# Kernel tuning notes

Measured on AMD Instinct MI355X. Metric: run time of the kernel, lower is better.

## Reference

```python
import math
import jax, jax.numpy as jnp
import numpy as np

B, T, N, F, H = 8, 16, 64, 64, 1024  # feature_dim must equal num_regions for the einsum to be valid


def _linear_init(key, out_dim, in_dim):
    kw, kb = jax.random.split(key)
    s = 1.0 / np.sqrt(in_dim)
    W = jax.random.uniform(kw, (out_dim, in_dim), jnp.float32, -s, s)
    b = jax.random.uniform(kb, (out_dim,), jnp.float32, -s, s)
    return W, b


def setup_inputs() -> dict:
    key = jax.random.key(0)
    k0, k1, k2, k3, k4 = jax.random.split(key, 5)
    M = jax.random.normal(k0, (B, T, N, N, F), jnp.float32)
    Wo, bo = _linear_init(k1, H, N * F)      # origin_proj
    Wso, bso = _linear_init(k2, N, H)        # origin_score
    Wd, bd = _linear_init(k3, H, N * F)      # dest_proj
    Wsd, bsd = _linear_init(k4, N, H)        # dest_score
    return {"M": M, "Wo": Wo, "bo": bo, "Wso": Wso, "bso": bso,
            "Wd": Wd, "bd": bd, "Wsd": Wsd, "bsd": bsd}


def _sparse_attention(scores, u):
    # scores: (BT, N, N)
    p = jax.nn.softmax(scores, axis=-1)
    entropy = -jnp.sum(p * jnp.log(p + 1e-9), axis=-1)          # (BT, N)
    _, top_idx = jax.lax.top_k(-entropy, u)                      # u smallest-entropy rows
    bt = entropy.shape[0]
    mask = jnp.zeros(entropy.shape, bool).at[jnp.arange(bt)[:, None], top_idx].set(True)
    return p * mask[..., None]                                   # zero all but u rows


def reference(M, Wo, bo, Wso, bso, Wd, bd, Wsd, bsd):
    Bb, Tt, Nn, _, Ff = M.shape
    BT = Bb * Tt
    X = M.reshape(BT, Nn, Nn * Ff)                               # origin view
    Y = jnp.transpose(M, (0, 1, 3, 2, 4)).reshape(BT, Nn, Nn * Ff)  # dest view
    omega_scores = (X @ Wo.T + bo) @ Wso.T + bso                 # (BT, N, N)
    delta_scores = (Y @ Wd.T + bd) @ Wsd.T + bsd                 # (BT, N, N)
    u = max(1, int(math.log(Nn)))
    omega = _sparse_attention(omega_scores, u)
    delta = _sparse_attention(delta_scores, u)
    M_flat = M.reshape(BT, Nn, Nn, Ff)
    out = jnp.einsum('bij,bjkl->bikl', omega, M_flat)            # (BT, N, N, F)
    out = jnp.einsum('bikl,bjl->bijk', out, delta)               # requires F == N
    return out.reshape(Bb, Tt, Nn, Nn, Ff)
```

## Files before the change

kernel.cpp:

```cpp
#include <hip/hip_runtime.h>
#include <math.h>

#define NB 8
#define NT 16
#define NN 64
#define NF 64
#define NH 1024
#define BT 128
#define NFK 4096

typedef float  f32x4 __attribute__((ext_vector_type(4)));
typedef short  s16x8 __attribute__((ext_vector_type(8)));

#define MFMA_B16(a, b, c) __builtin_amdgcn_mfma_f32_16x16x32_bf16(a, b, c, 0, 0, 0)

#define BEFF_FOFF   524288
#define PSEL_FOFF   524416
#define RTAB_FOFF   589952
#define RES_FOFF    606336
#define DYN_FOFF    737408

__device__ __forceinline__ void split_bf16(float v, unsigned short& hi, unsigned short& lo) {
    unsigned u = __float_as_uint(v);
    float r = v - __uint_as_float(u & 0xFFFF0000u);
    hi = (unsigned short)(u >> 16);
    lo = (unsigned short)(__float_as_uint(r) >> 16);
}

__device__ __forceinline__ void split8(const float4& a0, const float4& a1, s16x8& ah, s16x8& al) {
    float fa[8];
    *(float4*)&fa[0] = a0; *(float4*)&fa[4] = a1;
    #pragma unroll
    for (int j = 0; j < 8; ++j) {
        unsigned u = __float_as_uint(fa[j]);
        float r = fa[j] - __uint_as_float(u & 0xFFFF0000u);
        ah[j] = (short)(u >> 16);
        al[j] = (short)(__float_as_uint(r) >> 16);
    }
}

__global__ __launch_bounds__(256) void fold_part(
    const float* __restrict__ Wso, const float* __restrict__ Wo,
    const float* __restrict__ Wsd, const float* __restrict__ Wd,
    float* __restrict__ fpart, int hchunk)
{
    const int which = blockIdx.y, kc = blockIdx.z;
    const float* __restrict__ A  = which ? Wsd : Wso;
    const float* __restrict__ Bm = which ? Wd  : Wo;
    const int c0 = blockIdx.x * 32;

    __shared__ float As[64][68];
    __shared__ float Bs[32][68];

    const int t = threadIdx.x;
    const int tx = t & 7, ty = t >> 3;

    float acc[2][4] = {};

    const int h0beg = kc * hchunk, h0end = h0beg + hchunk;
    for (int h0 = h0beg; h0 < h0end; h0 += 64) {
        #pragma unroll
        for (int it = 0; it < 4; ++it) {
            int r = (t >> 4) + it * 16, c4 = (t & 15) * 4;
            *(float4*)&As[r][c4] = *(const float4*)&A[r * NH + h0 + c4];
        }
        #pragma unroll
        for (int it = 0; it < 2; ++it) {
            int h = (t >> 3) + it * 32, cq = t & 7;
            float4 v = *(const float4*)&Bm[(size_t)(h0 + h) * NFK + c0 + cq * 4];
            Bs[cq * 4 + 0][h] = v.x; Bs[cq * 4 + 1][h] = v.y;
            Bs[cq * 4 + 2][h] = v.z; Bs[cq * 4 + 3][h] = v.w;
        }
        __syncthreads();
        #pragma unroll 4
        for (int kk = 0; kk < 64; kk += 4) {
            float4 a4[2], b4[4];
            a4[0] = *(const float4*)&As[ty][kk];
            a4[1] = *(const float4*)&As[ty + 32][kk];
            #pragma unroll
            for (int n = 0; n < 4; ++n) b4[n] = *(const float4*)&Bs[tx + 8 * n][kk];
            #pragma unroll
            for (int m = 0; m < 2; ++m)
                #pragma unroll
                for (int n = 0; n < 4; ++n)
                    acc[m][n] += a4[m].x * b4[n].x + a4[m].y * b4[n].y
                               + a4[m].z * b4[n].z + a4[m].w * b4[n].w;
        }
        __syncthreads();
    }
    float* __restrict__ outp = fpart + ((size_t)(kc * 2 + which) * 64) * NFK;
    #pragma unroll
    for (int m = 0; m < 2; ++m)
        #pragma unroll
        for (int n = 0; n < 4; ++n)
            outp[(size_t)(ty + 32 * m) * NFK + c0 + tx + 8 * n] = acc[m][n];
}

__global__ __launch_bounds__(256) void fold_reduce(
    const float* __restrict__ fpart, unsigned short* __restrict__ wfrag, int fcc)
{
    const int which = blockIdx.y;
    const int c0 = blockIdx.x * 64;
    const int t = threadIdx.x;
    const int r = t >> 2, cb = (t & 3) * 16;

    float s[16] = {};
    for (int c = 0; c < fcc; ++c) {
        const float* __restrict__ p =
            fpart + ((size_t)(c * 2 + which) * 64 + r) * NFK + c0 + cb;
        #pragma unroll
        for (int qq = 0; qq < 4; ++qq) {
            float4 v = *(const float4*)(p + 4 * qq);
            s[4 * qq + 0] += v.x; s[4 * qq + 1] += v.y;
            s[4 * qq + 2] += v.z; s[4 * qq + 3] += v.w;
        }
    }
    #pragma unroll
    for (int jj = 0; jj < 16; ++jj) {
        int c = c0 + cb + jj;
        unsigned short hi, lo;
        split_bf16(s[jj], hi, lo);
        int ct = r >> 4, lane = (((c >> 3) & 3) << 4) | (r & 15);
        int ks = c >> 5, j = c & 7;
        size_t offh = ((((size_t)(which * 2 + 0) * 4 + ct) * 128 + ks) * 64 + lane) * 8 + j;
        size_t offl = ((((size_t)(which * 2 + 1) * 4 + ct) * 128 + ks) * 64 + lane) * 8 + j;
        wfrag[offh] = hi;
        wfrag[offl] = lo;
    }
}

__global__ __launch_bounds__(256) void bias_kernel(
    const float* __restrict__ Wso, const float* __restrict__ bo, const float* __restrict__ bso,
    const float* __restrict__ Wsd, const float* __restrict__ bd, const float* __restrict__ bsd,
    float* __restrict__ beff)
{
    const int which = blockIdx.x;
    const float* __restrict__ Ws = which ? Wsd : Wso;
    const float* __restrict__ bb = which ? bd  : bo;
    const float* __restrict__ bs = which ? bsd : bso;
    const int t = threadIdx.x;
    const int r = t >> 2, c = t & 3;
    const float* wp = Ws + r * NH + c * 256;
    const float* bp = bb + c * 256;
    float s = 0.f;
    #pragma unroll 4
    for (int i = 0; i < 64; ++i) {
        float4 wv = *(const float4*)(wp + 4 * i);
        float4 bv = *(const float4*)(bp + 4 * i);
        s += wv.x * bv.x + wv.y * bv.y + wv.z * bv.z + wv.w * bv.w;
    }
    __shared__ float part[64][4];
    part[r][c] = s;
    __syncthreads();
    if (t < 64)
        beff[which * 64 + t] = bs[t] + part[t][0] + part[t][1] + part[t][2] + part[t][3];
}

__global__ __launch_bounds__(256) void scores_part(
    const float* __restrict__ M, const unsigned short* __restrict__ wfrag,
    float* __restrict__ spart, int ksc)
{
    const int bt = blockIdx.x, which = blockIdx.y, kc = blockIdx.z;
    const float* __restrict__ Mbt = M + (size_t)bt * NN * NN * NF;
    const int t = threadIdx.x;
    const int w = t >> 6, l = t & 63, q = l >> 4, ln = l & 15;
    const int arow = 16 * w + ln;

    const unsigned short* __restrict__ wfl = wfrag + (size_t)which * 524288 + (size_t)l * 8;
#define BOFF(part, ct, ks) ((((part) * 4 + (ct)) * 128 + (ks)) * 512)
#define AADDR(ks) (Mbt + q * 8 + ((which == 0) \
        ? (arow * NFK + (ks) * 32) \
        : ((((ks) >> 1) * NFK) + arow * 64 + (((ks) & 1) * 32))))

    const int ks0 = kc * ksc, ksend = ks0 + ksc;
    const int g0 = ks0 >> 2, gend = ksend >> 2;

    f32x4 acc[4];
    #pragma unroll
    for (int ct = 0; ct < 4; ++ct) acc[ct] = (f32x4)0.f;

    float4 Ac[4][2], An[4][2];
    #pragma unroll
    for (int kk = 0; kk < 4; ++kk) {
        const float* ap = AADDR(ks0 + kk);
        Ac[kk][0] = *(const float4*)ap;
        Ac[kk][1] = *(const float4*)(ap + 4);
    }
    s16x8 bhc[4], blc[4];
    #pragma unroll
    for (int ct = 0; ct < 4; ++ct) {
        bhc[ct] = *(const s16x8*)(wfl + BOFF(0, ct, ks0));
        blc[ct] = *(const s16x8*)(wfl + BOFF(1, ct, ks0));
    }

    for (int g = g0; g < gend; ++g) {
        if (g + 1 < gend) {
            #pragma unroll
            for (int kk = 0; kk < 4; ++kk) {
                const float* ap = AADDR(4 * (g + 1) + kk);
                An[kk][0] = *(const float4*)ap;
                An[kk][1] = *(const float4*)(ap + 4);
            }
        }
        #pragma unroll
        for (int kk = 0; kk < 4; ++kk) {
            const int ks = 4 * g + kk;
            s16x8 bhn[4], bln[4];
            const bool pf = (ks + 1 < ksend);
            if (pf) {
                #pragma unroll
                for (int ct = 0; ct < 4; ++ct) {
                    bhn[ct] = *(const s16x8*)(wfl + BOFF(0, ct, ks + 1));
                    bln[ct] = *(const s16x8*)(wfl + BOFF(1, ct, ks + 1));
                }
            }
            s16x8 ah, al;
            split8(Ac[kk][0], Ac[kk][1], ah, al);
            #pragma unroll
            for (int ct = 0; ct < 4; ++ct) {
                acc[ct] = MFMA_B16(ah, bhc[ct], acc[ct]);
                acc[ct] = MFMA_B16(al, bhc[ct], acc[ct]);
                acc[ct] = MFMA_B16(ah, blc[ct], acc[ct]);
            }
            if (pf) {
                #pragma unroll
                for (int ct = 0; ct < 4; ++ct) { bhc[ct] = bhn[ct]; blc[ct] = bln[ct]; }
            }
        }
        #pragma unroll
        for (int kk = 0; kk < 4; ++kk) { Ac[kk][0] = An[kk][0]; Ac[kk][1] = An[kk][1]; }
    }
#undef AADDR
#undef BOFF

    float* __restrict__ pout = spart + ((size_t)(kc * 2 + which) * BT + bt) * 4096;
    #pragma unroll
    for (int ct = 0; ct < 4; ++ct)
        #pragma unroll
        for (int reg = 0; reg < 4; ++reg)
            pout[(16 * w + 4 * q + reg) * 64 + 16 * ct + ln] = acc[ct][reg];
}

__global__ __launch_bounds__(256) void finalize_kernel(
    const float* __restrict__ spart, const float* __restrict__ beff,
    float* __restrict__ psel, int* __restrict__ rtab, int scc)
{
    const int bt = blockIdx.x, which = blockIdx.y;
    const int t = threadIdx.x;
    const int row = t >> 2, cb = (t & 3) * 16;

    float s[16] = {};
    for (int c = 0; c < scc; ++c) {
        const float* __restrict__ p =
            spart + ((size_t)(c * 2 + which) * BT + bt) * 4096 + row * 64 + cb;
        #pragma unroll
        for (int qq = 0; qq < 4; ++qq) {
            float4 v = *(const float4*)(p + 4 * qq);
            s[4 * qq + 0] += v.x; s[4 * qq + 1] += v.y;
            s[4 * qq + 2] += v.z; s[4 * qq + 3] += v.w;
        }
    }
    #pragma unroll
    for (int jj = 0; jj < 16; ++jj) s[jj] += beff[which * 64 + cb + jj];

    float m = -INFINITY;
    #pragma unroll
    for (int jj = 0; jj < 16; ++jj) m = fmaxf(m, s[jj]);
    m = fmaxf(m, __shfl_xor(m, 1));
    m = fmaxf(m, __shfl_xor(m, 2));

    float e[16], sum = 0.f;
    #pragma unroll
    for (int jj = 0; jj < 16; ++jj) { e[jj] = expf(s[jj] - m); sum += e[jj]; }
    sum += __shfl_xor(sum, 1);
    sum += __shfl_xor(sum, 2);
    const float inv = 1.0f / sum;

    float pv[16], h = 0.f;
    #pragma unroll
    for (int jj = 0; jj < 16; ++jj) {
        pv[jj] = e[jj] * inv;
        h += pv[jj] * logf(pv[jj] + 1e-9f);
    }
    h += __shfl_xor(h, 1);
    h += __shfl_xor(h, 2);
    const float H = -h;

    __shared__ float ent[64];
    __shared__ int sel[4];
    if ((t & 3) == 0) ent[row] = H;
    __syncthreads();
    if (t == 0) {
        unsigned long long used = 0ull;
        for (int ss = 0; ss < 4; ++ss) {
            float best = INFINITY; int bi = 0;
            for (int r = 0; r < 64; ++r) {
                if ((used >> r) & 1ull) continue;
                if (ent[r] < best) { best = ent[r]; bi = r; }
            }
            used |= 1ull << bi;
            sel[ss] = bi;
        }
    }
    __syncthreads();

    int* __restrict__ rt = rtab + ((size_t)which * BT + bt) * 64;
    if (t < 64) rt[t] = -1;
    __syncthreads();
    if (t < 4) rt[sel[t]] = t;

    #pragma unroll
    for (int ss = 0; ss < 4; ++ss) {
        if (row == sel[ss]) {
            float* __restrict__ dp = psel + (((size_t)which * BT + bt) * 4 + ss) * 64 + cb;
            #pragma unroll
            for (int jj = 0; jj < 16; ++jj) dp[jj] = pv[jj];
        }
    }
}

__global__ __launch_bounds__(256) void res_compute(
    const float* __restrict__ M, const float* __restrict__ psel,
    float* __restrict__ resb)
{
    const int bt = blockIdx.x, kc = blockIdx.y;
    __shared__ float po[4][64], pd[4][64];
    __shared__ float o1[4][16][68];

    const int t = threadIdx.x;
    {
        int ss = t >> 6, l = t & 63;
        po[ss][l] = psel[(((size_t)0 * BT + bt) * 4 + ss) * 64 + l];
        pd[ss][l] = psel[(((size_t)1 * BT + bt) * 4 + ss) * 64 + l];
    }
    __syncthreads();

    const float* __restrict__ Ms = M + (size_t)bt * NN * NFK + kc * 1024 + t * 4;

    float4 a0 = {0,0,0,0}, a1 = {0,0,0,0}, a2 = {0,0,0,0}, a3 = {0,0,0,0};
    #pragma unroll 4
    for (int j = 0; j < NN; ++j) {
        float4 mv = *(const float4*)(Ms + (size_t)j * NFK);
        float w0 = po[0][j], w1 = po[1][j], w2 = po[2][j], w3 = po[3][j];
        a0.x += w0 * mv.x; a0.y += w0 * mv.y; a0.z += w0 * mv.z; a0.w += w0 * mv.w;
        a1.x += w1 * mv.x; a1.y += w1 * mv.y; a1.z += w1 * mv.z; a1.w += w1 * mv.w;
        a2.x += w2 * mv.x; a2.y += w2 * mv.y; a2.z += w2 * mv.z; a2.w += w2 * mv.w;
        a3.x += w3 * mv.x; a3.y += w3 * mv.y; a3.z += w3 * mv.z; a3.w += w3 * mv.w;
    }
    {
        int kl = t >> 4, l4 = (t & 15) * 4;
        *(float4*)&o1[0][kl][l4] = a0;
        *(float4*)&o1[1][kl][l4] = a1;
        *(float4*)&o1[2][kl][l4] = a2;
        *(float4*)&o1[3][kl][l4] = a3;
    }
    __syncthreads();
    {
        int i = t >> 6, jj = (t >> 4) & 3, k = t & 15;
        float v = 0.f;
        #pragma unroll
        for (int l4 = 0; l4 < 16; ++l4) {
            float4 ov = *(const float4*)&o1[i][k][l4 * 4];
            float4 pvv = *(const float4*)&pd[jj][l4 * 4];
            v += ov.x * pvv.x + ov.y * pvv.y + ov.z * pvv.z + ov.w * pvv.w;
        }
        resb[(((size_t)bt * 4 + i) * 4 + jj) * 64 + kc * 16 + k] = v;
    }
}

__global__ __launch_bounds__(256) void writer_kernel(
    const float* __restrict__ resb, const int* __restrict__ rtab,
    float* __restrict__ out)
{
    const int b = blockIdx.x, bt = b >> 6, i = b & 63;
    const int t = threadIdx.x;
    __shared__ float rl[4][64];

    const int ii = rtab[((size_t)0 * BT + bt) * 64 + i];
    const int jd = rtab[((size_t)1 * BT + bt) * 64 + (t >> 2)];
    if (ii >= 0)
        rl[t >> 6][t & 63] = resb[(((size_t)bt * 4 + ii) * 4 + (t >> 6)) * 64 + (t & 63)];
    __syncthreads();

    float4 v0 = {0,0,0,0}, v1 = {0,0,0,0}, v2 = {0,0,0,0}, v3 = {0,0,0,0};
    if (ii >= 0 && jd >= 0) {
        const int kb = (t & 3) * 16;
        v0 = *(const float4*)&rl[jd][kb + 0];
        v1 = *(const float4*)&rl[jd][kb + 4];
        v2 = *(const float4*)&rl[jd][kb + 8];
        v3 = *(const float4*)&rl[jd][kb + 12];
    }
    float* __restrict__ dst = out + (size_t)b * 4096 + t * 16;
    *(float4*)(dst + 0)  = v0;
    *(float4*)(dst + 4)  = v1;
    *(float4*)(dst + 8)  = v2;
    *(float4*)(dst + 12) = v3;
}

extern "C" void kernel_launch(void* const* d_in, const int* in_sizes, int n_in,
                              void* d_out, int out_size, void* d_ws, size_t ws_size,
                              hipStream_t stream)
{
    const float* M   = (const float*)d_in[0];
    const float* Wo  = (const float*)d_in[1];
    const float* bo  = (const float*)d_in[2];
    const float* Wso = (const float*)d_in[3];
    const float* bso = (const float*)d_in[4];
    const float* Wd  = (const float*)d_in[5];
    const float* bd  = (const float*)d_in[6];
    const float* Wsd = (const float*)d_in[7];
    const float* bsd = (const float*)d_in[8];
    float* out = (float*)d_out;

    float* ws = (float*)d_ws;
    unsigned short* wfrag = (unsigned short*)d_ws;
    float* beff = ws + BEFF_FOFF;
    float* psel = ws + PSEL_FOFF;
    int*   rtab = (int*)(ws + RTAB_FOFF);
    float* resb = ws + RES_FOFF;

    int FCC = 2, SCC = 4;
    {
        size_t need = ((size_t)DYN_FOFF + (size_t)FCC * 524288 + (size_t)SCC * 1048576) * 4;
        if (ws_size < need) { FCC = 1; SCC = 1; }
    }
    float* fpart = ws + DYN_FOFF;
    float* spart = fpart + (size_t)FCC * 524288;

    fold_part<<<dim3(128, 2, FCC), 256, 0, stream>>>(Wso, Wo, Wsd, Wd, fpart, NH / FCC);
    bias_kernel<<<2, 256, 0, stream>>>(Wso, bo, bso, Wsd, bd, bsd, beff);
    fold_reduce<<<dim3(64, 2), 256, 0, stream>>>(fpart, wfrag, FCC);
    scores_part<<<dim3(BT, 2, SCC), 256, 0, stream>>>(M, wfrag, spart, 128 / SCC);
    finalize_kernel<<<dim3(BT, 2), 256, 0, stream>>>(spart, beff, psel, rtab, SCC);
    res_compute<<<dim3(BT, 4), 256, 0, stream>>>(M, psel, resb);
    writer_kernel<<<BT * 64, 256, 0, stream>>>(resb, rtab, out);
}
```

Before: 405.7 us.

## Stage folded weights in LDS, split res_compute over j, fuse bias kernel

```diff
diff --git a/kernel.cpp b/kernel.cpp
--- a/kernel.cpp
+++ b/kernel.cpp
@@ -18,7 +18,7 @@
 #define PSEL_FOFF   524416
 #define RTAB_FOFF   589952
 #define RES_FOFF    606336
-#define DYN_FOFF    737408
+#define DYN_FOFF    868480
 
 __device__ __forceinline__ void split_bf16(float v, unsigned short& hi, unsigned short& lo) {
     unsigned u = __float_as_uint(v);
@@ -97,7 +97,10 @@
 }
 
 __global__ __launch_bounds__(256) void fold_reduce(
-    const float* __restrict__ fpart, unsigned short* __restrict__ wfrag, int fcc)
+    const float* __restrict__ fpart, unsigned short* __restrict__ wfrag, int fcc,
+    const float* __restrict__ Wso, const float* __restrict__ bo, const float* __restrict__ bso,
+    const float* __restrict__ Wsd, const float* __restrict__ bd, const float* __restrict__ bsd,
+    float* __restrict__ beff)
 {
     const int which = blockIdx.y;
     const int c0 = blockIdx.x * 64;
@@ -127,111 +130,120 @@
         wfrag[offh] = hi;
         wfrag[offl] = lo;
     }
-}
-
-__global__ __launch_bounds__(256) void bias_kernel(
-    const float* __restrict__ Wso, const float* __restrict__ bo, const float* __restrict__ bso,
-    const float* __restrict__ Wsd, const float* __restrict__ bd, const float* __restrict__ bsd,
-    float* __restrict__ beff)
-{
-    const int which = blockIdx.x;
-    const float* __restrict__ Ws = which ? Wsd : Wso;
-    const float* __restrict__ bb = which ? bd  : bo;
-    const float* __restrict__ bs = which ? bsd : bso;
-    const int t = threadIdx.x;
-    const int r = t >> 2, c = t & 3;
-    const float* wp = Ws + r * NH + c * 256;
-    const float* bp = bb + c * 256;
-    float s = 0.f;
-    #pragma unroll 4
-    for (int i = 0; i < 64; ++i) {
-        float4 wv = *(const float4*)(wp + 4 * i);
-        float4 bv = *(const float4*)(bp + 4 * i);
-        s += wv.x * bv.x + wv.y * bv.y + wv.z * bv.z + wv.w * bv.w;
-    }
-    __shared__ float part[64][4];
-    part[r][c] = s;
-    __syncthreads();
-    if (t < 64)
-        beff[which * 64 + t] = bs[t] + part[t][0] + part[t][1] + part[t][2] + part[t][3];
-}
+
+    if (blockIdx.x == 0) {
+        const float* __restrict__ Ws = which ? Wsd : Wso;
+        const float* __restrict__ bb = which ? bd  : bo;
+        const float* __restrict__ bs = which ? bsd : bso;
+        const int r2 = t >> 2, c2 = t & 3;
+        const float* wp = Ws + r2 * NH + c2 * 256;
+        const float* bp = bb + c2 * 256;
+        float sacc = 0.f;
+        #pragma unroll 4
+        for (int i2 = 0; i2 < 64; ++i2) {
+            float4 wv = *(const float4*)(wp + 4 * i2);
+            float4 bv = *(const float4*)(bp + 4 * i2);
+            sacc += wv.x * bv.x + wv.y * bv.y + wv.z * bv.z + wv.w * bv.w;
+        }
+        __shared__ float part[64][4];
+        part[r2][c2] = sacc;
+        __syncthreads();
+        if (t < 64)
+            beff[which * 64 + t] = bs[t] + part[t][0] + part[t][1] + part[t][2] + part[t][3];
+    }
+}
+
+#define CHUNK(fid, ks) ((size_t)((fid) * 128 + (ks)) * 512)
 
 __global__ __launch_bounds__(256) void scores_part(
     const float* __restrict__ M, const unsigned short* __restrict__ wfrag,
     float* __restrict__ spart, int ksc)
 {
     const int bt = blockIdx.x, which = blockIdx.y, kc = blockIdx.z;
-    const float* __restrict__ Mbt = M + (size_t)bt * NN * NN * NF;
+    const float* __restrict__ Mbt = M + (size_t)bt * NN * NFK;
     const int t = threadIdx.x;
     const int w = t >> 6, l = t & 63, q = l >> 4, ln = l & 15;
     const int arow = 16 * w + ln;
 
-    const unsigned short* __restrict__ wfl = wfrag + (size_t)which * 524288 + (size_t)l * 8;
-#define BOFF(part, ct, ks) ((((part) * 4 + (ct)) * 128 + (ks)) * 512)
+    __shared__ unsigned short Bsh[2][4][8][512];
+
+    const unsigned short* __restrict__ wbase = wfrag + (size_t)which * 524288;
+
 #define AADDR(ks) (Mbt + q * 8 + ((which == 0) \
         ? (arow * NFK + (ks) * 32) \
         : ((((ks) >> 1) * NFK) + arow * 64 + (((ks) & 1) * 32))))
 
-    const int ks0 = kc * ksc, ksend = ks0 + ksc;
-    const int g0 = ks0 >> 2, gend = ksend >> 2;
+    const int ks0 = kc * ksc;
+    const int ngroups = ksc >> 2;
 
     f32x4 acc[4];
     #pragma unroll
     for (int ct = 0; ct < 4; ++ct) acc[ct] = (f32x4)0.f;
 
     float4 Ac[4][2], An[4][2];
+    s16x8 Bn[8];
+
     #pragma unroll
     for (int kk = 0; kk < 4; ++kk) {
         const float* ap = AADDR(ks0 + kk);
         Ac[kk][0] = *(const float4*)ap;
         Ac[kk][1] = *(const float4*)(ap + 4);
-    }
-    s16x8 bhc[4], blc[4];
-    #pragma unroll
-    for (int ct = 0; ct < 4; ++ct) {
-        bhc[ct] = *(const s16x8*)(wfl + BOFF(0, ct, ks0));
-        blc[ct] = *(const s16x8*)(wfl + BOFF(1, ct, ks0));
-    }
-
-    for (int g = g0; g < gend; ++g) {
-        if (g + 1 < gend) {
+        #pragma unroll
+        for (int ii = 0; ii < 2; ++ii)
+            Bn[kk * 2 + ii] = *(const s16x8*)(wbase + CHUNK(w + ii * 4, ks0 + kk) + l * 8);
+    }
+    #pragma unroll
+    for (int kk = 0; kk < 4; ++kk)
+        #pragma unroll
+        for (int ii = 0; ii < 2; ++ii)
+            *(s16x8*)&Bsh[0][kk][w + ii * 4][l * 8] = Bn[kk * 2 + ii];
+    __syncthreads();
+
+    int cur = 0;
+    for (int g = 0; g < ngroups; ++g) {
+        const bool more = (g + 1 < ngroups);
+        const int ksn = ks0 + (g + 1) * 4;
+        if (more) {
             #pragma unroll
             for (int kk = 0; kk < 4; ++kk) {
-                const float* ap = AADDR(4 * (g + 1) + kk);
+                const float* ap = AADDR(ksn + kk);
                 An[kk][0] = *(const float4*)ap;
                 An[kk][1] = *(const float4*)(ap + 4);
+                #pragma unroll
+                for (int ii = 0; ii < 2; ++ii)
+                    Bn[kk * 2 + ii] = *(const s16x8*)(wbase + CHUNK(w + ii * 4, ksn + kk) + l * 8);
             }
         }
         #pragma unroll
         for (int kk = 0; kk < 4; ++kk) {
-            const int ks = 4 * g + kk;
-            s16x8 bhn[4], bln[4];
-            const bool pf = (ks + 1 < ksend);
-            if (pf) {
-                #pragma unroll
-                for (int ct = 0; ct < 4; ++ct) {
-                    bhn[ct] = *(const s16x8*)(wfl + BOFF(0, ct, ks + 1));
-                    bln[ct] = *(const s16x8*)(wfl + BOFF(1, ct, ks + 1));
-                }
+            s16x8 bh[4], bl[4];
+            #pragma unroll
+            for (int ct = 0; ct < 4; ++ct) {
+                bh[ct] = *(const s16x8*)&Bsh[cur][kk][ct][l * 8];
+                bl[ct] = *(const s16x8*)&Bsh[cur][kk][4 + ct][l * 8];
             }
             s16x8 ah, al;
             split8(Ac[kk][0], Ac[kk][1], ah, al);
             #pragma unroll
             for (int ct = 0; ct < 4; ++ct) {
-                acc[ct] = MFMA_B16(ah, bhc[ct], acc[ct]);
-                acc[ct] = MFMA_B16(al, bhc[ct], acc[ct]);
-                acc[ct] = MFMA_B16(ah, blc[ct], acc[ct]);
+                acc[ct] = MFMA_B16(ah, bh[ct], acc[ct]);
+                acc[ct] = MFMA_B16(al, bh[ct], acc[ct]);
+                acc[ct] = MFMA_B16(ah, bl[ct], acc[ct]);
             }
-            if (pf) {
+        }
+        if (more) {
+            #pragma unroll
+            for (int kk = 0; kk < 4; ++kk)
                 #pragma unroll
-                for (int ct = 0; ct < 4; ++ct) { bhc[ct] = bhn[ct]; blc[ct] = bln[ct]; }
-            }
-        }
-        #pragma unroll
-        for (int kk = 0; kk < 4; ++kk) { Ac[kk][0] = An[kk][0]; Ac[kk][1] = An[kk][1]; }
+                for (int ii = 0; ii < 2; ++ii)
+                    *(s16x8*)&Bsh[cur ^ 1][kk][w + ii * 4][l * 8] = Bn[kk * 2 + ii];
+            #pragma unroll
+            for (int kk = 0; kk < 4; ++kk) { Ac[kk][0] = An[kk][0]; Ac[kk][1] = An[kk][1]; }
+            __syncthreads();
+            cur ^= 1;
+        }
     }
 #undef AADDR
-#undef BOFF
 
     float* __restrict__ pout = spart + ((size_t)(kc * 2 + which) * BT + bt) * 4096;
     #pragma unroll
@@ -321,27 +333,29 @@
 
 __global__ __launch_bounds__(256) void res_compute(
     const float* __restrict__ M, const float* __restrict__ psel,
-    float* __restrict__ resb)
-{
-    const int bt = blockIdx.x, kc = blockIdx.y;
+    float* __restrict__ resb2)
+{
+    const int bt = blockIdx.x, kc = blockIdx.y, jh = blockIdx.z;
     __shared__ float po[4][64], pd[4][64];
     __shared__ float o1[4][16][68];
 
     const int t = threadIdx.x;
     {
-        int ss = t >> 6, l = t & 63;
-        po[ss][l] = psel[(((size_t)0 * BT + bt) * 4 + ss) * 64 + l];
-        pd[ss][l] = psel[(((size_t)1 * BT + bt) * 4 + ss) * 64 + l];
-    }
-    __syncthreads();
-
-    const float* __restrict__ Ms = M + (size_t)bt * NN * NFK + kc * 1024 + t * 4;
+        int ss = t >> 6, ll = t & 63;
+        po[ss][ll] = psel[(((size_t)0 * BT + bt) * 4 + ss) * 64 + ll];
+        pd[ss][ll] = psel[(((size_t)1 * BT + bt) * 4 + ss) * 64 + ll];
+    }
+    __syncthreads();
+
+    const float* __restrict__ Ms =
+        M + (size_t)bt * NN * NFK + (size_t)(jh * 32) * NFK + kc * 1024 + t * 4;
 
     float4 a0 = {0,0,0,0}, a1 = {0,0,0,0}, a2 = {0,0,0,0}, a3 = {0,0,0,0};
-    #pragma unroll 4
-    for (int j = 0; j < NN; ++j) {
+    #pragma unroll 8
+    for (int j = 0; j < 32; ++j) {
         float4 mv = *(const float4*)(Ms + (size_t)j * NFK);
-        float w0 = po[0][j], w1 = po[1][j], w2 = po[2][j], w3 = po[3][j];
+        int jg = jh * 32 + j;
+        float w0 = po[0][jg], w1 = po[1][jg], w2 = po[2][jg], w3 = po[3][jg];
         a0.x += w0 * mv.x; a0.y += w0 * mv.y; a0.z += w0 * mv.z; a0.w += w0 * mv.w;
         a1.x += w1 * mv.x; a1.y += w1 * mv.y; a1.z += w1 * mv.z; a1.w += w1 * mv.w;
         a2.x += w2 * mv.x; a2.y += w2 * mv.y; a2.z += w2 * mv.z; a2.w += w2 * mv.w;
@@ -364,37 +378,40 @@
             float4 pvv = *(const float4*)&pd[jj][l4 * 4];
             v += ov.x * pvv.x + ov.y * pvv.y + ov.z * pvv.z + ov.w * pvv.w;
         }
-        resb[(((size_t)bt * 4 + i) * 4 + jj) * 64 + kc * 16 + k] = v;
+        resb2[((((size_t)jh * BT + bt) * 4 + i) * 4 + jj) * 64 + kc * 16 + k] = v;
     }
 }
 
 __global__ __launch_bounds__(256) void writer_kernel(
-    const float* __restrict__ resb, const int* __restrict__ rtab,
+    const float* __restrict__ resb2, const int* __restrict__ rtab,
     float* __restrict__ out)
 {
     const int b = blockIdx.x, bt = b >> 6, i = b & 63;
     const int t = threadIdx.x;
     __shared__ float rl[4][64];
-
-    const int ii = rtab[((size_t)0 * BT + bt) * 64 + i];
-    const int jd = rtab[((size_t)1 * BT + bt) * 64 + (t >> 2)];
-    if (ii >= 0)
-        rl[t >> 6][t & 63] = resb[(((size_t)bt * 4 + ii) * 4 + (t >> 6)) * 64 + (t & 63)];
-    __syncthreads();
-
-    float4 v0 = {0,0,0,0}, v1 = {0,0,0,0}, v2 = {0,0,0,0}, v3 = {0,0,0,0};
-    if (ii >= 0 && jd >= 0) {
-        const int kb = (t & 3) * 16;
-        v0 = *(const float4*)&rl[jd][kb + 0];
-        v1 = *(const float4*)&rl[jd][kb + 4];
-        v2 = *(const float4*)&rl[jd][kb + 8];
-        v3 = *(const float4*)&rl[jd][kb + 12];
-    }
-    float* __restrict__ dst = out + (size_t)b * 4096 + t * 16;
-    *(float4*)(dst + 0)  = v0;
-    *(float4*)(dst + 4)  = v1;
-    *(float4*)(dst + 8)  = v2;
-    *(float4*)(dst + 12) = v3;
+    __shared__ int jdl[64];
+
+    const int ii = rtab[(size_t)bt * 64 + i];
+    if (t < 64) jdl[t] = rtab[(size_t)BT * 64 + (size_t)bt * 64 + t];
+    if (ii >= 0) {
+        int jj = t >> 6, k = t & 63;
+        size_t base = (((size_t)bt * 4 + ii) * 4 + jj) * 64 + k;
+        rl[jj][k] = resb2[base] + resb2[(size_t)BT * 4 * 4 * 64 + base];
+    }
+    __syncthreads();
+
+    float* __restrict__ dst = out + (size_t)b * 4096;
+    #pragma unroll
+    for (int s = 0; s < 4; ++s) {
+        int p = s * 1024 + t * 4;
+        int jj = p >> 6, k = p & 63;
+        float4 v = {0.f, 0.f, 0.f, 0.f};
+        if (ii >= 0) {
+            int jd = jdl[jj];
+            if (jd >= 0) v = *(const float4*)&rl[jd][k];
+        }
+        *(float4*)(dst + p) = v;
+    }
 }
 
 extern "C" void kernel_launch(void* const* d_in, const int* in_sizes, int n_in,
@@ -414,10 +431,10 @@
 
     float* ws = (float*)d_ws;
     unsigned short* wfrag = (unsigned short*)d_ws;
-    float* beff = ws + BEFF_FOFF;
-    float* psel = ws + PSEL_FOFF;
-    int*   rtab = (int*)(ws + RTAB_FOFF);
-    float* resb = ws + RES_FOFF;
+    float* beff  = ws + BEFF_FOFF;
+    float* psel  = ws + PSEL_FOFF;
+    int*   rtab  = (int*)(ws + RTAB_FOFF);
+    float* resb2 = ws + RES_FOFF;
 
     int FCC = 2, SCC = 4;
     {
@@ -428,10 +445,10 @@
     float* spart = fpart + (size_t)FCC * 524288;
 
     fold_part<<<dim3(128, 2, FCC), 256, 0, stream>>>(Wso, Wo, Wsd, Wd, fpart, NH / FCC);
-    bias_kernel<<<2, 256, 0, stream>>>(Wso, bo, bso, Wsd, bd, bsd, beff);
-    fold_reduce<<<dim3(64, 2), 256, 0, stream>>>(fpart, wfrag, FCC);
+    fold_reduce<<<dim3(64, 2), 256, 0, stream>>>(fpart, wfrag, FCC,
+                                                 Wso, bo, bso, Wsd, bd, bsd, beff);
     scores_part<<<dim3(BT, 2, SCC), 256, 0, stream>>>(M, wfrag, spart, 128 / SCC);
     finalize_kernel<<<dim3(BT, 2), 256, 0, stream>>>(spart, beff, psel, rtab, SCC);
-    res_compute<<<dim3(BT, 4), 256, 0, stream>>>(M, psel, resb);
-    writer_kernel<<<BT * 64, 256, 0, stream>>>(resb, rtab, out);
-}
+    res_compute<<<dim3(BT, 4, 2), 256, 0, stream>>>(M, psel, resb2);
+    writer_kernel<<<BT * 64, 256, 0, stream>>>(resb2, rtab, out);
+}
```

Measured after the change: 378.8 us. -6.6%, faster.
